# Kernel tuning notes

Measured on AMD Instinct MI355X. Metric: run time of the kernel, lower is better.

The kernel has to match this reference:

```python
import jax, jax.numpy as jnp
import numpy as np

EMBED_DIM = 1024
NUM_HEADS = 16
HEAD_DIM = EMBED_DIM // NUM_HEADS


def setup_inputs() -> dict:
    key = jax.random.key(0)
    ks = jax.random.split(key, 10)
    s = 1.0 / np.sqrt(EMBED_DIM)
    x = jax.random.normal(ks[0], (2, 2048, EMBED_DIM), dtype=jnp.float32)
    Wq = jax.random.uniform(ks[1], (EMBED_DIM, EMBED_DIM), jnp.float32, -s, s)
    bq = jax.random.uniform(ks[2], (EMBED_DIM,), jnp.float32, -s, s)
    Wk = jax.random.uniform(ks[3], (EMBED_DIM, EMBED_DIM), jnp.float32, -s, s)
    bk = jax.random.uniform(ks[4], (EMBED_DIM,), jnp.float32, -s, s)
    Wv = jax.random.uniform(ks[5], (EMBED_DIM, EMBED_DIM), jnp.float32, -s, s)
    bv = jax.random.uniform(ks[6], (EMBED_DIM,), jnp.float32, -s, s)
    Wo = jax.random.uniform(ks[7], (EMBED_DIM, EMBED_DIM), jnp.float32, -s, s)
    bo = jax.random.uniform(ks[8], (EMBED_DIM,), jnp.float32, -s, s)
    return {"x": x, "Wq": Wq, "bq": bq, "Wk": Wk, "bk": bk,
            "Wv": Wv, "bv": bv, "Wo": Wo, "bo": bo}


def reference(x, Wq, bq, Wk, bk, Wv, bv, Wo, bo):
    b, s, e = x.shape
    h, d = NUM_HEADS, HEAD_DIM
    scale = d ** -0.5
    # projections (torch Linear: x @ W.T + b; here W stored as [in, out])
    q = (x @ Wq + bq).reshape(b, s, h, d)
    k = (x @ Wk + bk).reshape(b, s, h, d)
    v = (x @ Wv + bv).reshape(b, s, h, d)
    logits = jnp.einsum('bqhd,bkhd->bhqk', q, k) * scale
    causal = jnp.tril(jnp.ones((s, s), dtype=bool))  # keep lower triangle
    logits = jnp.where(causal, logits, -jnp.inf)
    attn = jax.nn.softmax(logits, axis=-1)
    out = jnp.einsum('bhqk,bkhd->bqhd', attn, v).reshape(b, s, e)
    return out @ Wo + bo
```

## Files before the change

kernel.cpp:

```cpp
#include <hip/hip_runtime.h>


#define EMB 1024
#define SEQ 2048
#define NB 2
#define NH 16
#define HD 64

#define QSCALE 0.18033688011112042f

typedef float f32x4 __attribute__((ext_vector_type(4)));
typedef float floatx4 __attribute__((ext_vector_type(4)));
typedef short short8 __attribute__((ext_vector_type(8)));
typedef __bf16 bf16x8 __attribute__((ext_vector_type(8)));
typedef unsigned short ushortx4 __attribute__((ext_vector_type(4)));
typedef unsigned int uintx4 __attribute__((ext_vector_type(4)));

__device__ __forceinline__ unsigned short f2bf(float f) {
  unsigned u = __builtin_bit_cast(unsigned, f);
  u += 0x7fffu + ((u >> 16) & 1u);
  return (unsigned short)(u >> 16);
}

__device__ __forceinline__ unsigned pkbf(float lo, float hi) {
  return ((unsigned)f2bf(hi) << 16) | (unsigned)f2bf(lo);
}

__device__ __forceinline__ f32x4 mfma16(short8 a, short8 b, f32x4 c) {
  return __builtin_amdgcn_mfma_f32_16x16x32_bf16(
      __builtin_bit_cast(bf16x8, a), __builtin_bit_cast(bf16x8, b), c, 0, 0, 0);
}

__device__ __forceinline__ void gload16(const void* g, void* lds) {
  __builtin_amdgcn_global_load_lds(
      (const __attribute__((address_space(1))) unsigned int*)g,
      (__attribute__((address_space(3))) unsigned int*)lds, 16, 0, 0);
}

__global__ __launch_bounds__(256) void cvt_x_kernel(
    const float* __restrict__ x, unsigned short* __restrict__ out) {
  const int idx = (blockIdx.x * 256 + threadIdx.x) * 4;
  floatx4 v = *(const floatx4*)(x + idx);
  ushortx4 o;
  #pragma unroll
  for (int i = 0; i < 4; ++i) o[i] = f2bf(v[i]);
  *(ushortx4*)(out + idx) = o;
}

__global__ __launch_bounds__(256) void cvt_wt_kernel(
    const float* __restrict__ W, unsigned short* __restrict__ WT) {
  __shared__ unsigned short tile[32][33];
  const int k0 = blockIdx.x * 32, n0 = blockIdx.y * 32;
  const int t = threadIdx.x;
  const int r = t >> 3, c = (t & 7) * 4;
  floatx4 v = *(const floatx4*)(W + (k0 + r) * EMB + n0 + c);
  #pragma unroll
  for (int i = 0; i < 4; ++i) tile[r][c + i] = f2bf(v[i]);
  __syncthreads();
  ushortx4 o;
  #pragma unroll
  for (int i = 0; i < 4; ++i) o[i] = tile[c + i][r];
  *(ushortx4*)(WT + (n0 + r) * EMB + k0 + c) = o;
}

__global__ __launch_bounds__(256) void gemm_qkv_kernel(
    const unsigned short* __restrict__ Xb,
    const unsigned short* __restrict__ W0, const unsigned short* __restrict__ W1,
    const unsigned short* __restrict__ W2,
    const float* __restrict__ b0, const float* __restrict__ b1,
    const float* __restrict__ b2,
    unsigned short* __restrict__ Qo, unsigned short* __restrict__ Ko,
    unsigned short* __restrict__ Vo) {
  __shared__ __align__(16) unsigned short As[128 * 64];
  __shared__ __align__(16) unsigned short Bs[128 * 64];
  const int z = blockIdx.z;
  const unsigned short* Wt = (z == 0) ? W0 : ((z == 1) ? W1 : W2);
  const float* bias = (z == 0) ? b0 : ((z == 1) ? b1 : b2);
  const float osc = (z == 0) ? QSCALE : 1.0f;
  const int m0 = blockIdx.y * 128, n0 = blockIdx.x * 128;
  const int tid = threadIdx.x, l = tid & 63, w = tid >> 6;
  const int g = l >> 4, ln = l & 15;
  const int wr = w >> 1, wc = w & 1;

  f32x4 acc[4][4];
  #pragma unroll
  for (int i = 0; i < 4; ++i)
    #pragma unroll
    for (int j = 0; j < 4; ++j) acc[i][j] = (f32x4){0.f, 0.f, 0.f, 0.f};

  for (int kt = 0; kt < 16; ++kt) {
    const int kb = kt * 64;
    #pragma unroll
    for (int it = 0; it < 4; ++it) {
      const int chunk = w * 4 + it;
      const int lin = chunk * 64 + l;
      const int row = lin >> 3, col = (lin & 7) * 8;
      gload16(Xb + (m0 + row) * EMB + kb + col, (char*)As + chunk * 1024);
      gload16(Wt + (n0 + row) * EMB + kb + col, (char*)Bs + chunk * 1024);
    }
    __syncthreads();
    #pragma unroll
    for (int kk = 0; kk < 64; kk += 32) {
      short8 a[4], b[4];
      #pragma unroll
      for (int i = 0; i < 4; ++i)
        a[i] = *(const short8*)(As + (wr * 64 + i * 16 + ln) * 64 + kk + g * 8);
      #pragma unroll
      for (int j = 0; j < 4; ++j)
        b[j] = *(const short8*)(Bs + (wc * 64 + j * 16 + ln) * 64 + kk + g * 8);
      #pragma unroll
      for (int i = 0; i < 4; ++i)
        #pragma unroll
        for (int j = 0; j < 4; ++j)
          acc[i][j] = mfma16(a[i], b[j], acc[i][j]);
    }
    __syncthreads();
  }

  const int mb = m0 + wr * 64, nb = n0 + wc * 64;
  #pragma unroll
  for (int j = 0; j < 4; ++j) {
    const int n = nb + j * 16 + ln;
    const float bgain = bias[n];
    const int h = n >> 6, d = n & 63;
    #pragma unroll
    for (int i = 0; i < 4; ++i) {
      const int mf = mb + i * 16 + 4 * g;
      const int bb = mf >> 11, ss = mf & 2047;
      if (z == 2) {
        ushortx4 o;
        #pragma unroll
        for (int e = 0; e < 4; ++e) o[e] = f2bf(acc[i][j][e] + bgain);
        *(ushortx4*)(Vo + ((bb * NH + h) * HD + d) * SEQ + ss) = o;
      } else {
        unsigned short* dst = (z == 0) ? Qo : Ko;
        const int base = ((bb * NH + h) * SEQ + ss) * HD + d;
        #pragma unroll
        for (int e = 0; e < 4; ++e)
          dst[base + e * HD] = f2bf((acc[i][j][e] + bgain) * osc);
      }
    }
  }
}

__global__ __launch_bounds__(256) void attn_kernel(
    const unsigned short* __restrict__ Q, const unsigned short* __restrict__ K,
    const unsigned short* __restrict__ Vt, unsigned short* __restrict__ O) {
  __shared__ __align__(16) unsigned short Kt[2][64 * 64];
  __shared__ __align__(16) unsigned short Vl[2][64 * 64];
  const int tpair = blockIdx.x, h = blockIdx.y, b = blockIdx.z;
  const int tid = threadIdx.x, l = tid & 63, w = tid >> 6;
  const int g = l >> 4, ln = l & 15;
  const int bh = b * NH + h;
  const size_t baseQK = (size_t)bh * SEQ * HD;
  const size_t baseV = (size_t)bh * HD * SEQ;
  const int xr = ln & 7;
  const int srcA = ((g & 1) << 5) + ln;
  const int srcB = srcA + 16;
  const bool hi = (g >> 1) != 0;

  const int st_row0 = (w * 2 * 64 + l) >> 3, st_c0 = ((w * 2) * 64 + l) & 7;
  const int st_row1 = ((w * 2 + 1) * 64 + l) >> 3, st_c1 = ((w * 2 + 1) * 64 + l) & 7;
  const int st_csw0 = st_c0 ^ (st_row0 & 7);
  const int st_csw1 = st_c1 ^ (st_row1 & 7);

  #pragma unroll 1
  for (int pass = 0; pass < 2; ++pass) {
    const int qt = (pass == 0) ? (31 - tpair) : tpair;
    const int nkt = qt + 1;
    const int q0 = qt * 64, qw = q0 + w * 16;

    {
      gload16(K + baseQK + (size_t)(0 * 64 + st_row0) * HD + st_csw0 * 8,
              (char*)&Kt[0][0] + (w * 2) * 1024);
      gload16(Vt + baseV + (size_t)st_row0 * SEQ + 0 * 64 + st_csw0 * 8,
              (char*)&Vl[0][0] + (w * 2) * 1024);
      gload16(K + baseQK + (size_t)(0 * 64 + st_row1) * HD + st_csw1 * 8,
              (char*)&Kt[0][0] + (w * 2 + 1) * 1024);
      gload16(Vt + baseV + (size_t)st_row1 * SEQ + 0 * 64 + st_csw1 * 8,
              (char*)&Vl[0][0] + (w * 2 + 1) * 1024);
    }

    const int qrow = qw + ln;
    short8 qf0 = *(const short8*)(Q + baseQK + (size_t)qrow * HD + g * 8);
    short8 qf1 = *(const short8*)(Q + baseQK + (size_t)qrow * HD + 32 + g * 8);

    float m_run = -1e30f, l_run = 0.f;
    f32x4 acc[4];
    #pragma unroll
    for (int dj = 0; dj < 4; ++dj) acc[dj] = (f32x4){0.f, 0.f, 0.f, 0.f};

    #pragma unroll 1
    for (int kt = 0; kt < nkt; ++kt) {
      const int cur = kt & 1;
      const bool has_next = (kt + 1 < nkt);
      if (has_next) {
        const int nb = cur ^ 1;
        const int kn = kt + 1;
        gload16(K + baseQK + (size_t)(kn * 64 + st_row0) * HD + st_csw0 * 8,
                (char*)&Kt[nb][0] + (w * 2) * 1024);
        gload16(Vt + baseV + (size_t)st_row0 * SEQ + kn * 64 + st_csw0 * 8,
                (char*)&Vl[nb][0] + (w * 2) * 1024);
        gload16(K + baseQK + (size_t)(kn * 64 + st_row1) * HD + st_csw1 * 8,
                (char*)&Kt[nb][0] + (w * 2 + 1) * 1024);
        gload16(Vt + baseV + (size_t)st_row1 * SEQ + kn * 64 + st_csw1 * 8,
                (char*)&Vl[nb][0] + (w * 2 + 1) * 1024);
        asm volatile("s_waitcnt vmcnt(4)" ::: "memory");
      } else {
        asm volatile("s_waitcnt vmcnt(0)" ::: "memory");
      }
      __builtin_amdgcn_s_barrier();

      const bool diag = (kt == qt);
      const int jmax = diag ? w : 3;

      f32x4 sv[4];
      #pragma unroll
      for (int j = 0; j < 4; ++j)
        sv[j] = (f32x4){-1e30f, -1e30f, -1e30f, -1e30f};
      #pragma unroll
      for (int j = 0; j < 4; ++j) {
        if (j <= jmax) {
          f32x4 t = (f32x4){0.f, 0.f, 0.f, 0.f};
          short8 kf0 = *(const short8*)(
              &Kt[cur][(j * 16 + ln) * 64 + ((g ^ xr) * 8)]);
          t = mfma16(kf0, qf0, t);
          short8 kf1 = *(const short8*)(
              &Kt[cur][(j * 16 + ln) * 64 + (((4 + g) ^ xr) * 8)]);
          t = mfma16(kf1, qf1, t);
          if (diag && j == w) {
            #pragma unroll
            for (int e = 0; e < 4; ++e)
              sv[j][e] = (4 * g + e <= ln) ? t[e] : -1e30f;
          } else {
            sv[j] = t;
          }
        }
      }

      float tm = -1e30f;
      #pragma unroll
      for (int j = 0; j < 4; ++j)
        #pragma unroll
        for (int e = 0; e < 4; ++e) tm = fmaxf(tm, sv[j][e]);
      tm = fmaxf(tm, __shfl_xor(tm, 16));
      tm = fmaxf(tm, __shfl_xor(tm, 32));
      const float nm = fmaxf(m_run, tm);
      const float al = exp2f(m_run - nm);
      m_run = nm;

      float p[4][4];
      float rs = 0.f;
      #pragma unroll
      for (int j = 0; j < 4; ++j)
        #pragma unroll
        for (int e = 0; e < 4; ++e) {
          p[j][e] = exp2f(sv[j][e] - nm);
          rs += p[j][e];
        }
      rs += __shfl_xor(rs, 16);
      rs += __shfl_xor(rs, 32);
      l_run = l_run * al + rs;
      #pragma unroll
      for (int dj = 0; dj < 4; ++dj) acc[dj] *= al;

      unsigned pk[4][2];
      #pragma unroll
      for (int j = 0; j < 4; ++j) {
        pk[j][0] = pkbf(p[j][0], p[j][1]);
        pk[j][1] = pkbf(p[j][2], p[j][3]);
      }

      const int ksmax = (diag && w < 2) ? 1 : 2;
      short8 pf0, pf1;
      {
        unsigned a0 = __shfl(pk[0][0], srcA), a1 = __shfl(pk[0][1], srcA);
        unsigned a2 = __shfl(pk[0][0], srcB), a3 = __shfl(pk[0][1], srcB);
        unsigned b0 = __shfl(pk[1][0], srcA), b1 = __shfl(pk[1][1], srcA);
        unsigned b2 = __shfl(pk[1][0], srcB), b3 = __shfl(pk[1][1], srcB);
        uintx4 u;
        u[0] = hi ? b0 : a0; u[1] = hi ? b1 : a1;
        u[2] = hi ? b2 : a2; u[3] = hi ? b3 : a3;
        pf0 = __builtin_bit_cast(short8, u);
      }
      if (ksmax > 1) {
        unsigned a0 = __shfl(pk[2][0], srcA), a1 = __shfl(pk[2][1], srcA);
        unsigned a2 = __shfl(pk[2][0], srcB), a3 = __shfl(pk[2][1], srcB);
        unsigned b0 = __shfl(pk[3][0], srcA), b1 = __shfl(pk[3][1], srcA);
        unsigned b2 = __shfl(pk[3][0], srcB), b3 = __shfl(pk[3][1], srcB);
        uintx4 u;
        u[0] = hi ? b0 : a0; u[1] = hi ? b1 : a1;
        u[2] = hi ? b2 : a2; u[3] = hi ? b3 : a3;
        pf1 = __builtin_bit_cast(short8, u);
      }

      #pragma unroll
      for (int dj = 0; dj < 4; ++dj) {
        short8 vb0 = *(const short8*)(
            &Vl[cur][(dj * 16 + ln) * 64 + ((g ^ xr) * 8)]);
        acc[dj] = mfma16(vb0, pf0, acc[dj]);
        if (ksmax > 1) {
          short8 vb1 = *(const short8*)(
              &Vl[cur][(dj * 16 + ln) * 64 + (((4 + g) ^ xr) * 8)]);
          acc[dj] = mfma16(vb1, pf1, acc[dj]);
        }
      }

      asm volatile("" ::: "memory");
      __builtin_amdgcn_s_barrier();
    }

    const float inv = 1.f / l_run;
    const size_t orow = ((size_t)b * SEQ + qw + ln) * EMB + h * HD;
    #pragma unroll
    for (int dj = 0; dj < 4; ++dj) {
      ushortx4 o;
      #pragma unroll
      for (int e = 0; e < 4; ++e) o[e] = f2bf(acc[dj][e] * inv);
      *(ushortx4*)(O + orow + dj * 16 + 4 * g) = o;
    }
  }
}

__global__ __launch_bounds__(256) void gemm_o_kernel(
    const unsigned short* __restrict__ Ab, const unsigned short* __restrict__ Wt,
    const float* __restrict__ bias, float* __restrict__ out) {
  __shared__ __align__(16) unsigned short As[128 * 64];
  __shared__ __align__(16) unsigned short Bs[128 * 64];
  const int m0 = blockIdx.y * 128, n0 = blockIdx.x * 128;
  const int tid = threadIdx.x, l = tid & 63, w = tid >> 6;
  const int g = l >> 4, ln = l & 15;
  const int wr = w >> 1, wc = w & 1;

  f32x4 acc[4][4];
  #pragma unroll
  for (int i = 0; i < 4; ++i)
    #pragma unroll
    for (int j = 0; j < 4; ++j) acc[i][j] = (f32x4){0.f, 0.f, 0.f, 0.f};

  for (int kt = 0; kt < 16; ++kt) {
    const int kb = kt * 64;
    #pragma unroll
    for (int it = 0; it < 4; ++it) {
      const int chunk = w * 4 + it;
      const int lin = chunk * 64 + l;
      const int row = lin >> 3, col = (lin & 7) * 8;
      gload16(Ab + (m0 + row) * EMB + kb + col, (char*)As + chunk * 1024);
      gload16(Wt + (n0 + row) * EMB + kb + col, (char*)Bs + chunk * 1024);
    }
    __syncthreads();
    #pragma unroll
    for (int kk = 0; kk < 64; kk += 32) {
      short8 a[4], b[4];
      #pragma unroll
      for (int i = 0; i < 4; ++i)
        a[i] = *(const short8*)(As + (wr * 64 + i * 16 + ln) * 64 + kk + g * 8);
      #pragma unroll
      for (int j = 0; j < 4; ++j)
        b[j] = *(const short8*)(Bs + (wc * 64 + j * 16 + ln) * 64 + kk + g * 8);
      #pragma unroll
      for (int i = 0; i < 4; ++i)
        #pragma unroll
        for (int j = 0; j < 4; ++j)
          acc[i][j] = mfma16(a[i], b[j], acc[i][j]);
    }
    __syncthreads();
  }

  const int mb = m0 + wr * 64, nb = n0 + wc * 64;
  #pragma unroll
  for (int j = 0; j < 4; ++j) {
    const int n = nb + j * 16 + ln;
    const float bgain = bias[n];
    #pragma unroll
    for (int i = 0; i < 4; ++i) {
      #pragma unroll
      for (int e = 0; e < 4; ++e) {
        const int m = mb + i * 16 + 4 * g + e;
        out[m * EMB + n] = acc[i][j][e] + bgain;
      }
    }
  }
}

extern "C" void kernel_launch(void* const* d_in, const int* in_sizes, int n_in,
                              void* d_out, int out_size, void* d_ws, size_t ws_size,
                              hipStream_t stream) {
  const float* x  = (const float*)d_in[0];
  const float* Wq = (const float*)d_in[1];
  const float* bq = (const float*)d_in[2];
  const float* Wk = (const float*)d_in[3];
  const float* bk = (const float*)d_in[4];
  const float* Wv = (const float*)d_in[5];
  const float* bv = (const float*)d_in[6];
  const float* Wo = (const float*)d_in[7];
  const float* bo = (const float*)d_in[8];
  float* out = (float*)d_out;

  char* ws = (char*)d_ws;
  unsigned short* Xb  = (unsigned short*)(ws);
  unsigned short* WqT = (unsigned short*)(ws + 8388608);
  unsigned short* WkT = (unsigned short*)(ws + 10485760);
  unsigned short* WvT = (unsigned short*)(ws + 12582912);
  unsigned short* WoT = (unsigned short*)(ws + 14680064);
  unsigned short* Qb  = (unsigned short*)(ws + 16777216);
  unsigned short* Kb  = (unsigned short*)(ws + 25165824);
  unsigned short* Vtb = (unsigned short*)(ws + 33554432);
  unsigned short* Ao  = Xb;

  hipLaunchKernelGGL(cvt_x_kernel, dim3(4096), dim3(256), 0, stream, x, Xb);
  hipLaunchKernelGGL(cvt_wt_kernel, dim3(32, 32), dim3(256), 0, stream, Wq, WqT);
  hipLaunchKernelGGL(cvt_wt_kernel, dim3(32, 32), dim3(256), 0, stream, Wk, WkT);
  hipLaunchKernelGGL(cvt_wt_kernel, dim3(32, 32), dim3(256), 0, stream, Wv, WvT);
  hipLaunchKernelGGL(cvt_wt_kernel, dim3(32, 32), dim3(256), 0, stream, Wo, WoT);
  hipLaunchKernelGGL(gemm_qkv_kernel, dim3(8, 32, 3), dim3(256), 0, stream,
                     Xb, WqT, WkT, WvT, bq, bk, bv, Qb, Kb, Vtb);
  hipLaunchKernelGGL(attn_kernel, dim3(16, 16, 2), dim3(256), 0, stream,
                     Qb, Kb, Vtb, Ao);
  hipLaunchKernelGGL(gemm_o_kernel, dim3(8, 32), dim3(256), 0, stream,
                     Ao, WoT, bo, out);
}
```

Measured before the change: 181.8 us.

## Merge weight conversions, swap MFMA operands for vector stores, add setprio and hardware bf16 casts

The four weight transpose-convert launches are merged into a single launch with a z dimension. The Q/K projection and the output GEMM swap MFMA operand order so each lane holds four consecutive columns, which turns scalar strided stores into 8- or 16-byte vector stores with vector bias loads. The attention kernel raises wave priority around its MFMA sections, and the manual round-to-nearest-even bf16 conversion is replaced with compiler __bf16 casts. The cost is a duplicated k-loop branch in the QKV GEMM, which adds code size.

```diff
diff --git a/kernel.cpp b/kernel.cpp
--- a/kernel.cpp
+++ b/kernel.cpp
@@ -13,17 +13,20 @@
 typedef float floatx4 __attribute__((ext_vector_type(4)));
 typedef short short8 __attribute__((ext_vector_type(8)));
 typedef __bf16 bf16x8 __attribute__((ext_vector_type(8)));
+typedef __bf16 bf16x2 __attribute__((ext_vector_type(2)));
 typedef unsigned short ushortx4 __attribute__((ext_vector_type(4)));
 typedef unsigned int uintx4 __attribute__((ext_vector_type(4)));
 
-__device__ __forceinline__ unsigned short f2bf(float f) {
-  unsigned u = __builtin_bit_cast(unsigned, f);
-  u += 0x7fffu + ((u >> 16) & 1u);
-  return (unsigned short)(u >> 16);
+__device__ __forceinline__ unsigned short bf16u(float f) {
+  __bf16 h = (__bf16)f;
+  return __builtin_bit_cast(unsigned short, h);
 }
 
 __device__ __forceinline__ unsigned pkbf(float lo, float hi) {
-  return ((unsigned)f2bf(hi) << 16) | (unsigned)f2bf(lo);
+  bf16x2 v;
+  v[0] = (__bf16)lo;
+  v[1] = (__bf16)hi;
+  return __builtin_bit_cast(unsigned, v);
 }
 
 __device__ __forceinline__ f32x4 mfma16(short8 a, short8 b, f32x4 c) {
@@ -43,25 +46,47 @@
   floatx4 v = *(const floatx4*)(x + idx);
   ushortx4 o;
   #pragma unroll
-  for (int i = 0; i < 4; ++i) o[i] = f2bf(v[i]);
+  for (int i = 0; i < 4; ++i) o[i] = bf16u(v[i]);
   *(ushortx4*)(out + idx) = o;
 }
 
-__global__ __launch_bounds__(256) void cvt_wt_kernel(
-    const float* __restrict__ W, unsigned short* __restrict__ WT) {
+__global__ __launch_bounds__(256) void cvt_w4_kernel(
+    const float* __restrict__ W0, const float* __restrict__ W1,
+    const float* __restrict__ W2, const float* __restrict__ W3,
+    unsigned short* __restrict__ T0, unsigned short* __restrict__ T1,
+    unsigned short* __restrict__ T2, unsigned short* __restrict__ T3) {
   __shared__ unsigned short tile[32][33];
+  const int z = blockIdx.z;
+  const float* W = (z == 0) ? W0 : (z == 1) ? W1 : (z == 2) ? W2 : W3;
+  unsigned short* WT = (z == 0) ? T0 : (z == 1) ? T1 : (z == 2) ? T2 : T3;
   const int k0 = blockIdx.x * 32, n0 = blockIdx.y * 32;
   const int t = threadIdx.x;
   const int r = t >> 3, c = (t & 7) * 4;
   floatx4 v = *(const floatx4*)(W + (k0 + r) * EMB + n0 + c);
   #pragma unroll
-  for (int i = 0; i < 4; ++i) tile[r][c + i] = f2bf(v[i]);
+  for (int i = 0; i < 4; ++i) tile[r][c + i] = bf16u(v[i]);
   __syncthreads();
   ushortx4 o;
   #pragma unroll
   for (int i = 0; i < 4; ++i) o[i] = tile[c + i][r];
   *(ushortx4*)(WT + (n0 + r) * EMB + k0 + c) = o;
 }
+
+#define GEMM_KLOOP(OP1, OP2)                                                 \
+    for (int kk = 0; kk < 64; kk += 32) {                                    \
+      short8 a[4], b[4];                                                     \
+      _Pragma("unroll")                                                      \
+      for (int i = 0; i < 4; ++i)                                            \
+        a[i] = *(const short8*)(As + (wr * 64 + i * 16 + ln) * 64 + kk + g * 8); \
+      _Pragma("unroll")                                                      \
+      for (int j = 0; j < 4; ++j)                                            \
+        b[j] = *(const short8*)(Bs + (wc * 64 + j * 16 + ln) * 64 + kk + g * 8); \
+      _Pragma("unroll")                                                      \
+      for (int i = 0; i < 4; ++i)                                            \
+        _Pragma("unroll")                                                    \
+        for (int j = 0; j < 4; ++j)                                          \
+          acc[i][j] = mfma16(OP1, OP2, acc[i][j]);                           \
+    }
 
 __global__ __launch_bounds__(256) void gemm_qkv_kernel(
     const unsigned short* __restrict__ Xb,
@@ -76,7 +101,7 @@
   const int z = blockIdx.z;
   const unsigned short* Wt = (z == 0) ? W0 : ((z == 1) ? W1 : W2);
   const float* bias = (z == 0) ? b0 : ((z == 1) ? b1 : b2);
-  const float osc = (z == 0) ? QSCALE : 1.0f;
+  const bool sw = (z != 2);
   const int m0 = blockIdx.y * 128, n0 = blockIdx.x * 128;
   const int tid = threadIdx.x, l = tid & 63, w = tid >> 6;
   const int g = l >> 4, ln = l & 15;
@@ -99,45 +124,47 @@
       gload16(Wt + (n0 + row) * EMB + kb + col, (char*)Bs + chunk * 1024);
     }
     __syncthreads();
-    #pragma unroll
-    for (int kk = 0; kk < 64; kk += 32) {
-      short8 a[4], b[4];
-      #pragma unroll
-      for (int i = 0; i < 4; ++i)
-        a[i] = *(const short8*)(As + (wr * 64 + i * 16 + ln) * 64 + kk + g * 8);
-      #pragma unroll
-      for (int j = 0; j < 4; ++j)
-        b[j] = *(const short8*)(Bs + (wc * 64 + j * 16 + ln) * 64 + kk + g * 8);
-      #pragma unroll
-      for (int i = 0; i < 4; ++i)
-        #pragma unroll
-        for (int j = 0; j < 4; ++j)
-          acc[i][j] = mfma16(a[i], b[j], acc[i][j]);
+    if (sw) {
+      GEMM_KLOOP(b[j], a[i])
+    } else {
+      GEMM_KLOOP(a[i], b[j])
     }
     __syncthreads();
   }
 
   const int mb = m0 + wr * 64, nb = n0 + wc * 64;
-  #pragma unroll
-  for (int j = 0; j < 4; ++j) {
-    const int n = nb + j * 16 + ln;
-    const float bgain = bias[n];
-    const int h = n >> 6, d = n & 63;
-    #pragma unroll
-    for (int i = 0; i < 4; ++i) {
-      const int mf = mb + i * 16 + 4 * g;
-      const int bb = mf >> 11, ss = mf & 2047;
-      if (z == 2) {
+  if (sw) {
+    unsigned short* dst = (z == 0) ? Qo : Ko;
+    const float osc = (z == 0) ? QSCALE : 1.0f;
+    #pragma unroll
+    for (int j = 0; j < 4; ++j) {
+      const int n = nb + j * 16 + 4 * g;
+      floatx4 bv_ = *(const floatx4*)(bias + n);
+      const int h = n >> 6, d = n & 63;
+      #pragma unroll
+      for (int i = 0; i < 4; ++i) {
+        const int m = mb + i * 16 + ln;
+        const int bb = m >> 11, ss = m & 2047;
         ushortx4 o;
         #pragma unroll
-        for (int e = 0; e < 4; ++e) o[e] = f2bf(acc[i][j][e] + bgain);
+        for (int e = 0; e < 4; ++e) o[e] = bf16u((acc[i][j][e] + bv_[e]) * osc);
+        *(ushortx4*)(dst + ((bb * NH + h) * SEQ + ss) * HD + d) = o;
+      }
+    }
+  } else {
+    #pragma unroll
+    for (int j = 0; j < 4; ++j) {
+      const int n = nb + j * 16 + ln;
+      const float bgain = bias[n];
+      const int h = n >> 6, d = n & 63;
+      #pragma unroll
+      for (int i = 0; i < 4; ++i) {
+        const int mf = mb + i * 16 + 4 * g;
+        const int bb = mf >> 11, ss = mf & 2047;
+        ushortx4 o;
+        #pragma unroll
+        for (int e = 0; e < 4; ++e) o[e] = bf16u(acc[i][j][e] + bgain);
         *(ushortx4*)(Vo + ((bb * NH + h) * HD + d) * SEQ + ss) = o;
-      } else {
-        unsigned short* dst = (z == 0) ? Qo : Ko;
-        const int base = ((bb * NH + h) * SEQ + ss) * HD + d;
-        #pragma unroll
-        for (int e = 0; e < 4; ++e)
-          dst[base + e * HD] = f2bf((acc[i][j][e] + bgain) * osc);
       }
     }
   }
@@ -195,16 +222,16 @@
       const int cur = kt & 1;
       const bool has_next = (kt + 1 < nkt);
       if (has_next) {
-        const int nb = cur ^ 1;
+        const int nxt = cur ^ 1;
         const int kn = kt + 1;
         gload16(K + baseQK + (size_t)(kn * 64 + st_row0) * HD + st_csw0 * 8,
-                (char*)&Kt[nb][0] + (w * 2) * 1024);
+                (char*)&Kt[nxt][0] + (w * 2) * 1024);
         gload16(Vt + baseV + (size_t)st_row0 * SEQ + kn * 64 + st_csw0 * 8,
-                (char*)&Vl[nb][0] + (w * 2) * 1024);
+                (char*)&Vl[nxt][0] + (w * 2) * 1024);
         gload16(K + baseQK + (size_t)(kn * 64 + st_row1) * HD + st_csw1 * 8,
-                (char*)&Kt[nb][0] + (w * 2 + 1) * 1024);
+                (char*)&Kt[nxt][0] + (w * 2 + 1) * 1024);
         gload16(Vt + baseV + (size_t)st_row1 * SEQ + kn * 64 + st_csw1 * 8,
-                (char*)&Vl[nb][0] + (w * 2 + 1) * 1024);
+                (char*)&Vl[nxt][0] + (w * 2 + 1) * 1024);
         asm volatile("s_waitcnt vmcnt(4)" ::: "memory");
       } else {
         asm volatile("s_waitcnt vmcnt(0)" ::: "memory");
@@ -218,6 +245,7 @@
       #pragma unroll
       for (int j = 0; j < 4; ++j)
         sv[j] = (f32x4){-1e30f, -1e30f, -1e30f, -1e30f};
+      __builtin_amdgcn_s_setprio(1);
       #pragma unroll
       for (int j = 0; j < 4; ++j) {
         if (j <= jmax) {
@@ -237,6 +265,7 @@
           }
         }
       }
+      __builtin_amdgcn_s_setprio(0);
 
       float tm = -1e30f;
       #pragma unroll
@@ -294,6 +323,7 @@
         pf1 = __builtin_bit_cast(short8, u);
       }
 
+      __builtin_amdgcn_s_setprio(1);
       #pragma unroll
       for (int dj = 0; dj < 4; ++dj) {
         short8 vb0 = *(const short8*)(
@@ -305,6 +335,7 @@
           acc[dj] = mfma16(vb1, pf1, acc[dj]);
         }
       }
+      __builtin_amdgcn_s_setprio(0);
 
       asm volatile("" ::: "memory");
       __builtin_amdgcn_s_barrier();
@@ -316,7 +347,7 @@
     for (int dj = 0; dj < 4; ++dj) {
       ushortx4 o;
       #pragma unroll
-      for (int e = 0; e < 4; ++e) o[e] = f2bf(acc[dj][e] * inv);
+      for (int e = 0; e < 4; ++e) o[e] = bf16u(acc[dj][e] * inv);
       *(ushortx4*)(O + orow + dj * 16 + 4 * g) = o;
     }
   }
@@ -349,36 +380,20 @@
       gload16(Wt + (n0 + row) * EMB + kb + col, (char*)Bs + chunk * 1024);
     }
     __syncthreads();
-    #pragma unroll
-    for (int kk = 0; kk < 64; kk += 32) {
-      short8 a[4], b[4];
-      #pragma unroll
-      for (int i = 0; i < 4; ++i)
-        a[i] = *(const short8*)(As + (wr * 64 + i * 16 + ln) * 64 + kk + g * 8);
-      #pragma unroll
-      for (int j = 0; j < 4; ++j)
-        b[j] = *(const short8*)(Bs + (wc * 64 + j * 16 + ln) * 64 + kk + g * 8);
-      #pragma unroll
-      for (int i = 0; i < 4; ++i)
-        #pragma unroll
-        for (int j = 0; j < 4; ++j)
-          acc[i][j] = mfma16(a[i], b[j], acc[i][j]);
-    }
+    GEMM_KLOOP(b[j], a[i])
     __syncthreads();
   }
 
   const int mb = m0 + wr * 64, nb = n0 + wc * 64;
   #pragma unroll
   for (int j = 0; j < 4; ++j) {
-    const int n = nb + j * 16 + ln;
-    const float bgain = bias[n];
+    const int n = nb + j * 16 + 4 * g;
+    floatx4 bv_ = *(const floatx4*)(bias + n);
     #pragma unroll
     for (int i = 0; i < 4; ++i) {
-      #pragma unroll
-      for (int e = 0; e < 4; ++e) {
-        const int m = mb + i * 16 + 4 * g + e;
-        out[m * EMB + n] = acc[i][j][e] + bgain;
-      }
+      const int m = mb + i * 16 + ln;
+      floatx4 o = acc[i][j] + bv_;
+      *(floatx4*)(out + (size_t)m * EMB + n) = o;
     }
   }
 }
@@ -409,10 +424,8 @@
   unsigned short* Ao  = Xb;
 
   hipLaunchKernelGGL(cvt_x_kernel, dim3(4096), dim3(256), 0, stream, x, Xb);
-  hipLaunchKernelGGL(cvt_wt_kernel, dim3(32, 32), dim3(256), 0, stream, Wq, WqT);
-  hipLaunchKernelGGL(cvt_wt_kernel, dim3(32, 32), dim3(256), 0, stream, Wk, WkT);
-  hipLaunchKernelGGL(cvt_wt_kernel, dim3(32, 32), dim3(256), 0, stream, Wv, WvT);
-  hipLaunchKernelGGL(cvt_wt_kernel, dim3(32, 32), dim3(256), 0, stream, Wo, WoT);
+  hipLaunchKernelGGL(cvt_w4_kernel, dim3(32, 32, 4), dim3(256), 0, stream,
+                     Wq, Wk, Wv, Wo, WqT, WkT, WvT, WoT);
   hipLaunchKernelGGL(gemm_qkv_kernel, dim3(8, 32, 3), dim3(256), 0, stream,
                      Xb, WqT, WkT, WvT, bq, bk, bv, Qb, Kb, Vtb);
   hipLaunchKernelGGL(attn_kernel, dim3(16, 16, 2), dim3(256), 0, stream,
```

After: 174.0 us. -4.3%, faster.
